# Performance work log

Hardware: AMD Instinct MI355X
Metric: run time of the kernel (lower is better)

## Reference

```python
import jax, jax.numpy as jnp
import numpy as np

SPATIAL_SCALE = 0.25
N, C, H, W = 8, 256, 128, 128
P = 100000
IMG = 512.0  # image-space extent (H / spatial_scale)


def setup_inputs() -> dict:
    key = jax.random.key(0)
    k1, k2, k3, k4 = jax.random.split(key, 4)
    features = jax.random.normal(k1, (N, C, H, W), dtype=jnp.float32)
    batch_idx = jax.random.randint(k2, (P,), 0, N).astype(jnp.float32)
    xy = jax.random.uniform(k3, (P, 2), dtype=jnp.float32) * IMG
    rois = jnp.concatenate([batch_idx[:, None], xy], axis=1)  # [P,3]: (b, x, y)
    return {"features": features, "rois": rois}


def _interp(features, rois, spatial_scale):
    n, c, h, w = features.shape
    b = rois[:, 0].astype(jnp.int32)
    x = rois[:, 1] * spatial_scale
    y = rois[:, 2] * spatial_scale
    # RoIAlign-style bilinear interpolation with boundary handling
    valid = (y >= -1.0) & (y <= h) & (x >= -1.0) & (x <= w)
    y = jnp.maximum(y, 0.0)
    x = jnp.maximum(x, 0.0)
    y_low = jnp.floor(y).astype(jnp.int32)
    x_low = jnp.floor(x).astype(jnp.int32)
    y_at_edge = y_low >= h - 1
    x_at_edge = x_low >= w - 1
    y_low = jnp.minimum(y_low, h - 1)
    x_low = jnp.minimum(x_low, w - 1)
    y_high = jnp.where(y_at_edge, y_low, y_low + 1)
    x_high = jnp.where(x_at_edge, x_low, x_low + 1)
    y = jnp.where(y_at_edge, y_low.astype(y.dtype), y)
    x = jnp.where(x_at_edge, x_low.astype(x.dtype), x)
    ly = y - y_low
    lx = x - x_low
    hy = 1.0 - ly
    hx = 1.0 - lx
    w1 = (hy * hx)[:, None]  # [P,1]
    w2 = (hy * lx)[:, None]
    w3 = (ly * hx)[:, None]
    w4 = (ly * lx)[:, None]
    # fancy-index gather: [P, C] per corner
    v1 = features[b, :, y_low, x_low]
    v2 = features[b, :, y_low, x_high]
    v3 = features[b, :, y_high, x_low]
    v4 = features[b, :, y_high, x_high]
    out = w1 * v1 + w2 * v2 + w3 * v3 + w4 * v4  # [P, C]
    return jnp.where(valid[:, None], out, 0.0)


def reference(features, rois):
    return _interp(features, rois, SPATIAL_SCALE)
```

## Files before the change

### kernel.cpp

```cpp
#include <hip/hip_runtime.h>

#define SCALE   0.25f
#define NBATCH  8
#define CCH     256
#define HH      128
#define WW      128
#define HW      (HH * WW)
#define NBUCK   (NBATCH * HH)
#define CAP     160

#define CG      32
#define NCG     (CCH / CG)

typedef float f32x4 __attribute__((ext_vector_type(4)));


__global__ __launch_bounds__(1024) void k_bin(
    const float* __restrict__ rois, int* __restrict__ cnt,
    int4* __restrict__ slots, int P)
{
    __shared__ int lhist[NBUCK];
    __shared__ int lbase[NBUCK];
    const int t = threadIdx.x;
    lhist[t] = 0;
    __syncthreads();

    int p = blockIdx.x * 1024 + t;
    int mybk = -1, mypos = 0;
    int4 myrec = make_int4(0, 0, 0, 0);
    if (p < P) {
        float fb = rois[3 * p];
        float fx = rois[3 * p + 1] * SCALE;
        float fy = rois[3 * p + 2] * SCALE;
        int b = (int)fb;
        bool valid = (fy >= -1.0f) && (fy <= (float)HH) &&
                     (fx >= -1.0f) && (fx <= (float)WW);
        float y = fmaxf(fy, 0.0f);
        float x = fmaxf(fx, 0.0f);
        int ylo = (int)floorf(y);
        int xlo = (int)floorf(x);
        float yf = y, xf = x;
        int xhi;
        if (ylo >= HH - 1) { ylo = HH - 1; yf = (float)ylo; }
        if (xlo >= WW - 1) { xlo = WW - 1; xhi = WW - 1; xf = (float)xlo; }
        else               { xhi = xlo + 1; }
        float ly = yf - (float)ylo;
        float lx = xf - (float)xlo;
        unsigned pk = (unsigned)xlo | ((unsigned)xhi << 8) | (valid ? 0u : 0x80000000u);
        int bk = b * HH + ylo;
        mybk  = bk;
        mypos = atomicAdd(&lhist[bk], 1);
        myrec = make_int4(p, (int)pk, __float_as_int(lx), __float_as_int(ly));
    }
    __syncthreads();
    int h = lhist[t];
    lbase[t] = h ? atomicAdd(&cnt[t], h) : 0;
    __syncthreads();
    if (mybk >= 0) {
        int idx = lbase[mybk] + mypos;
        if (idx < CAP) slots[mybk * CAP + idx] = myrec;
    }
}

__global__ __launch_bounds__(512, 8) void k_main(
    const float* __restrict__ feat, const int4* __restrict__ slots,
    const int* __restrict__ cnt_arr, float* __restrict__ out)
{
    const int bk  = blockIdx.x & (NBUCK - 1);
    const int cgp = blockIdx.x >> 10;
    const int cnt = min(cnt_arr[bk], CAP);
    if (cnt == 0) return;
    const int b  = bk >> 7;
    const int yl = bk & 127;
    const int yh = min(yl + 1, HH - 1);

    __shared__ __align__(16) float4 lds4[2][WW][8];

    const int t    = threadIdx.x;
    const int wv   = t >> 6;
    const int lane = t & 63;
    const int sub  = lane >> 3;
    const int cq   = lane & 7;

    const int4* sb = slots + (size_t)bk * CAP;
    const int ii0 = wv * 8;
    int4 rc0 = sb[min(ii0 + sub, cnt - 1)];
    int4 rc1 = sb[min(ii0 + 64 + sub, cnt - 1)];

    {
        const int xq  = t & 31;
        const int cq8 = (t >> 5) & 7;
        const int row = t >> 8;
        const int y   = row ? yh : yl;
        const float* g = feat + ((size_t)(b * CCH + cgp * CG + 4 * cq8) * HH + y) * WW + 4 * xq;
        float4 f0 = *(const float4*)(g);
        float4 f1 = *(const float4*)(g + HW);
        float4 f2 = *(const float4*)(g + 2 * HW);
        float4 f3 = *(const float4*)(g + 3 * HW);
        float4* d = &lds4[row][4 * xq][(cq8 + xq) & 7];
        d[0]  = make_float4(f0.x, f1.x, f2.x, f3.x);
        d[8]  = make_float4(f0.y, f1.y, f2.y, f3.y);
        d[16] = make_float4(f0.z, f1.z, f2.z, f3.z);
        d[24] = make_float4(f0.w, f1.w, f2.w, f3.w);
    }
    __syncthreads();

    const float4* lo = &lds4[0][0][0];
    const float4* hi = &lds4[1][0][0];
    float* const outbase = out + cgp * CG + 4 * cq;

    auto process = [&](int4 r, bool act) {
        unsigned pk = (unsigned)r.y;
        float lx = __int_as_float(r.z);
        float ly = __int_as_float(r.w);
        float s  = ((int)pk < 0) ? 0.0f : 1.0f;
        float hy  = (1.0f - ly) * s;
        float lys = ly * s;
        float hx  = 1.0f - lx;
        float w1 = hy * hx, w2 = hy * lx, w3 = lys * hx, w4 = lys * lx;
        int xlo = pk & 255;
        int xhi = (pk >> 8) & 255;
        int alo = xlo * 8 + ((cq + (xlo >> 2)) & 7);
        int ahi = xhi * 8 + ((cq + (xhi >> 2)) & 7);
        float4 v1 = lo[alo], v2 = lo[ahi];
        float4 v3 = hi[alo], v4 = hi[ahi];
        f32x4 o;
        o.x = w1 * v1.x + w2 * v2.x + w3 * v3.x + w4 * v4.x;
        o.y = w1 * v1.y + w2 * v2.y + w3 * v3.y + w4 * v4.y;
        o.z = w1 * v1.z + w2 * v2.z + w3 * v3.z + w4 * v4.z;
        o.w = w1 * v1.w + w2 * v2.w + w3 * v3.w + w4 * v4.w;
        if (act)
            __builtin_nontemporal_store(o, (f32x4*)(outbase + (size_t)r.x * CCH));
    };

    process(rc0, ii0 + sub < cnt);
    if (ii0 + 64 < cnt)
        process(rc1, ii0 + 64 + sub < cnt);
    for (int ii = ii0 + 128; ii < cnt; ii += 64)
        process(sb[min(ii + sub, cnt - 1)], ii + sub < cnt);
}

extern "C" void kernel_launch(void* const* d_in, const int* in_sizes, int n_in,
                              void* d_out, int out_size, void* d_ws, size_t ws_size,
                              hipStream_t stream) {
    const float* feat = (const float*)d_in[0];
    const float* rois = (const float*)d_in[1];
    float* out = (float*)d_out;
    const int P = in_sizes[1] / 3;

    int*  cnt   = (int*)d_ws;
    int4* slots = (int4*)((char*)d_ws + NBUCK * sizeof(int));

    hipMemsetAsync(cnt, 0, NBUCK * sizeof(int), stream);
    const int bb = (P + 1023) / 1024;
    k_bin<<<bb, 1024, 0, stream>>>(rois, cnt, slots, P);
    k_main<<<NCG * NBUCK, 512, 0, stream>>>(feat, slots, cnt, out);
}
```

Before: 230.5 us.

## Merge adjacent row buckets per block to share feature rows; shrink binning blocks

```diff
diff --git a/kernel.cpp b/kernel.cpp
--- a/kernel.cpp
+++ b/kernel.cpp
@@ -15,17 +15,17 @@
 typedef float f32x4 __attribute__((ext_vector_type(4)));
 
 
-__global__ __launch_bounds__(1024) void k_bin(
+__global__ __launch_bounds__(256) void k_bin(
     const float* __restrict__ rois, int* __restrict__ cnt,
     int4* __restrict__ slots, int P)
 {
     __shared__ int lhist[NBUCK];
     __shared__ int lbase[NBUCK];
     const int t = threadIdx.x;
-    lhist[t] = 0;
+    for (int k = t; k < NBUCK; k += 256) lhist[k] = 0;
     __syncthreads();
 
-    int p = blockIdx.x * 1024 + t;
+    int p = blockIdx.x * 256 + t;
     int mybk = -1, mypos = 0;
     int4 myrec = make_int4(0, 0, 0, 0);
     if (p < P) {
@@ -53,8 +53,10 @@
         myrec = make_int4(p, (int)pk, __float_as_int(lx), __float_as_int(ly));
     }
     __syncthreads();
-    int h = lhist[t];
-    lbase[t] = h ? atomicAdd(&cnt[t], h) : 0;
+    for (int k = t; k < NBUCK; k += 256) {
+        int h = lhist[k];
+        lbase[k] = h ? atomicAdd(&cnt[k], h) : 0;
+    }
     __syncthreads();
     if (mybk >= 0) {
         int idx = lbase[mybk] + mypos;
@@ -62,19 +64,22 @@
     }
 }
 
-__global__ __launch_bounds__(512, 8) void k_main(
+__global__ __launch_bounds__(512, 6) void k_main(
     const float* __restrict__ feat, const int4* __restrict__ slots,
     const int* __restrict__ cnt_arr, float* __restrict__ out)
 {
-    const int bk  = blockIdx.x & (NBUCK - 1);
-    const int cgp = blockIdx.x >> 10;
-    const int cnt = min(cnt_arr[bk], CAP);
-    if (cnt == 0) return;
-    const int b  = bk >> 7;
-    const int yl = bk & 127;
-    const int yh = min(yl + 1, HH - 1);
+    const int bkp = blockIdx.x & 511;
+    const int cgp = blockIdx.x >> 9;
+    const int b   = bkp >> 6;
+    const int y0  = (bkp & 63) * 2;
+    const int bk0 = b * HH + y0;
 
-    __shared__ __align__(16) float4 lds4[2][WW][8];
+    const int n0 = min(cnt_arr[bk0], CAP);
+    const int n1 = min(cnt_arr[bk0 + 1], CAP);
+    const int tot = n0 + n1;
+    if (tot == 0) return;
+
+    __shared__ __align__(16) float4 lds4[3][WW][8];
 
     const int t    = threadIdx.x;
     const int wv   = t >> 6;
@@ -82,16 +87,20 @@
     const int sub  = lane >> 3;
     const int cq   = lane & 7;
 
-    const int4* sb = slots + (size_t)bk * CAP;
+    const int4* sb = slots + (size_t)bk0 * CAP;
     const int ii0 = wv * 8;
-    int4 rc0 = sb[min(ii0 + sub, cnt - 1)];
-    int4 rc1 = sb[min(ii0 + 64 + sub, cnt - 1)];
+    int j0 = min(ii0 + sub, tot - 1);        int q0 = j0 >= n0;
+    int j1 = min(ii0 + 64 + sub, tot - 1);   int q1 = j1 >= n0;
+    int j2 = min(ii0 + 128 + sub, tot - 1);  int q2 = j2 >= n0;
+    int4 rc0 = sb[q0 ? CAP + j0 - n0 : j0];
+    int4 rc1 = sb[q1 ? CAP + j1 - n0 : j1];
+    int4 rc2 = sb[q2 ? CAP + j2 - n0 : j2];
 
-    {
-        const int xq  = t & 31;
-        const int cq8 = (t >> 5) & 7;
-        const int row = t >> 8;
-        const int y   = row ? yh : yl;
+    for (int u = t; u < 768; u += 512) {
+        const int xq  = u & 31;
+        const int cq8 = (u >> 5) & 7;
+        const int row = u >> 8;
+        const int y   = min(y0 + row, HH - 1);
         const float* g = feat + ((size_t)(b * CCH + cgp * CG + 4 * cq8) * HH + y) * WW + 4 * xq;
         float4 f0 = *(const float4*)(g);
         float4 f1 = *(const float4*)(g + HW);
@@ -105,11 +114,9 @@
     }
     __syncthreads();
 
-    const float4* lo = &lds4[0][0][0];
-    const float4* hi = &lds4[1][0][0];
     float* const outbase = out + cgp * CG + 4 * cq;
 
-    auto process = [&](int4 r, bool act) {
+    auto process = [&](int4 r, int q, bool act) {
         unsigned pk = (unsigned)r.y;
         float lx = __int_as_float(r.z);
         float ly = __int_as_float(r.w);
@@ -122,6 +129,8 @@
         int xhi = (pk >> 8) & 255;
         int alo = xlo * 8 + ((cq + (xlo >> 2)) & 7);
         int ahi = xhi * 8 + ((cq + (xhi >> 2)) & 7);
+        const float4* lo = &lds4[q][0][0];
+        const float4* hi = lo + WW * 8;
         float4 v1 = lo[alo], v2 = lo[ahi];
         float4 v3 = hi[alo], v4 = hi[ahi];
         f32x4 o;
@@ -133,11 +142,14 @@
             __builtin_nontemporal_store(o, (f32x4*)(outbase + (size_t)r.x * CCH));
     };
 
-    process(rc0, ii0 + sub < cnt);
-    if (ii0 + 64 < cnt)
-        process(rc1, ii0 + 64 + sub < cnt);
-    for (int ii = ii0 + 128; ii < cnt; ii += 64)
-        process(sb[min(ii + sub, cnt - 1)], ii + sub < cnt);
+    process(rc0, q0, ii0 + sub < tot);
+    if (ii0 + 64 < tot)  process(rc1, q1, ii0 + 64 + sub < tot);
+    if (ii0 + 128 < tot) process(rc2, q2, ii0 + 128 + sub < tot);
+    for (int ii = ii0 + 192; ii < tot; ii += 64) {
+        int j = min(ii + sub, tot - 1);
+        int q = j >= n0;
+        process(sb[q ? CAP + j - n0 : j], q, ii + sub < tot);
+    }
 }
 
 extern "C" void kernel_launch(void* const* d_in, const int* in_sizes, int n_in,
@@ -152,7 +164,7 @@
     int4* slots = (int4*)((char*)d_ws + NBUCK * sizeof(int));
 
     hipMemsetAsync(cnt, 0, NBUCK * sizeof(int), stream);
-    const int bb = (P + 1023) / 1024;
-    k_bin<<<bb, 1024, 0, stream>>>(rois, cnt, slots, P);
-    k_main<<<NCG * NBUCK, 512, 0, stream>>>(feat, slots, cnt, out);
+    const int bb = (P + 255) / 256;
+    k_bin<<<bb, 256, 0, stream>>>(rois, cnt, slots, P);
+    k_main<<<NCG * NBATCH * (HH / 2), 512, 0, stream>>>(feat, slots, cnt, out);
 }
```

New measurement: 242.5 us. 1.05x slower.
